# Kernel optimization log

Measured on AMD Instinct MI355X. Metric: run time of the kernel, lower is better.

The kernel has to match this reference:

```python
import jax, jax.numpy as jnp
import numpy as np

B, T, H = 8, 2048, 1024
P = 64           # num_attention_project
N = 4096         # config.n (bias table length), N >= 2T-1
WINDOW = 64      # relative_attention
NEG = -10000.0


def setup_inputs() -> dict:
    key = jax.random.key(0)
    ks = jax.random.split(key, 10)
    s = 1.0 / np.sqrt(H)
    sp = 1.0 / np.sqrt(P)
    sb = 1.0 / np.sqrt(N)
    return {
        "attn_input": jax.random.normal(ks[0], (B, T, H), dtype=jnp.float32),
        "attention_mask": jnp.ones((B, T), dtype=jnp.float32),
        # Linear weights stored as [in, out] so y = x @ W + b
        "Wq": jax.random.uniform(ks[1], (H, P), minval=-s, maxval=s),
        "bq": jnp.zeros((P,), jnp.float32),
        "Wk": jax.random.uniform(ks[2], (H, P), minval=-s, maxval=s),
        "bk": jnp.zeros((P,), jnp.float32),
        "Wv": jax.random.uniform(ks[3], (H, P), minval=-s, maxval=s),
        "bv": jnp.zeros((P,), jnp.float32),
        "Wo": jax.random.uniform(ks[4], (P, H), minval=-sp, maxval=sp),
        "bo": jnp.zeros((H,), jnp.float32),
        "bias": jax.random.uniform(ks[5], (N,), minval=-sb, maxval=sb),
    }


def reference(attn_input, attention_mask, Wq, bq, Wk, bk, Wv, bv, Wo, bo, bias):
    q = attn_input @ Wq + bq            # [B,T,P]
    k = attn_input @ Wk + bk
    v = attn_input @ Wv + bv
    scores = jnp.einsum("btp,bsp->bts", q, k) / jnp.sqrt(jnp.float32(P))  # [B,T,T]
    # padding mask: note original broadcasts over COLUMNS via unsqueeze(-1)
    scores = scores + (1.0 - attention_mask)[:, :, None] * NEG
    # circulant window mask: keep |i-j| <= WINDOW (all ones if WINDOW >= T)
    i = jnp.arange(T)
    rel = i[:, None] - i[None, :]       # i - j
    win = (jnp.abs(rel) <= WINDOW) | (WINDOW >= T)
    scores = scores + jnp.where(win, 0.0, NEG)[None, :, :]
    # gathered learnable relative-position bias: bias[n//2 - i + j]
    scores = scores + bias[N // 2 - rel][None, :, :]
    attn = jax.nn.softmax(scores, axis=-1)
    out = jnp.einsum("bts,bsp->btp", attn, v)
    return out @ Wo + bo                # [B,T,H]
```

## Files before the change

kernel.cpp:

```cpp
#include <hip/hip_runtime.h>

using bf16x8 = __attribute__((ext_vector_type(8))) short;
using f32x4  = __attribute__((ext_vector_type(4))) float;

static __device__ inline unsigned short f2bf(float f) {
  unsigned int u = __float_as_uint(f);
  u += 0x7fffu + ((u >> 16) & 1u);
  return (unsigned short)(u >> 16);
}
static __device__ inline unsigned int pk2(float a, float b) {
  return (unsigned int)f2bf(a) | ((unsigned int)f2bf(b) << 16);
}

#define BAR_LGKM() { asm volatile("s_waitcnt lgkmcnt(0)" ::: "memory"); \
                     __builtin_amdgcn_sched_barrier(0); \
                     __builtin_amdgcn_s_barrier(); }

#define ROW16_MAX(x) { \
  { int _t = __builtin_amdgcn_update_dpp(0, __float_as_int(x), 0x121, 0xf, 0xf, true); x = fmaxf(x, __int_as_float(_t)); } \
  { int _t = __builtin_amdgcn_update_dpp(0, __float_as_int(x), 0x122, 0xf, 0xf, true); x = fmaxf(x, __int_as_float(_t)); } \
  { int _t = __builtin_amdgcn_update_dpp(0, __float_as_int(x), 0x124, 0xf, 0xf, true); x = fmaxf(x, __int_as_float(_t)); } \
  { int _t = __builtin_amdgcn_update_dpp(0, __float_as_int(x), 0x128, 0xf, 0xf, true); x = fmaxf(x, __int_as_float(_t)); } }
#define ROW16_SUM(x) { \
  { int _t = __builtin_amdgcn_update_dpp(0, __float_as_int(x), 0x121, 0xf, 0xf, true); x += __int_as_float(_t); } \
  { int _t = __builtin_amdgcn_update_dpp(0, __float_as_int(x), 0x122, 0xf, 0xf, true); x += __int_as_float(_t); } \
  { int _t = __builtin_amdgcn_update_dpp(0, __float_as_int(x), 0x124, 0xf, 0xf, true); x += __int_as_float(_t); } \
  { int _t = __builtin_amdgcn_update_dpp(0, __float_as_int(x), 0x128, 0xf, 0xf, true); x += __int_as_float(_t); } }

__global__ __launch_bounds__(256) void prep_kernel(
    const float* __restrict__ Wq, const float* __restrict__ Wk, const float* __restrict__ Wv,
    const float* __restrict__ Wo, const float* __restrict__ bq, const float* __restrict__ bk,
    const float* __restrict__ bv,
    unsigned short* __restrict__ Wt, unsigned short* __restrict__ Wot, float* __restrict__ bqkv)
{
  int idx = blockIdx.x * 256 + threadIdx.x;
  if (idx < 192 * 1024) {
    int n = idx >> 10, k = idx & 1023;
    const float* W = (n < 64) ? Wq : (n < 128) ? Wk : Wv;
    Wt[idx] = f2bf(W[k * 64 + (n & 63)]);
  } else if (idx < 192 * 1024 + 1024 * 64) {
    int j = idx - 192 * 1024;
    int n = j >> 6, k = j & 63;
    Wot[j] = f2bf(Wo[k * 1024 + n]);
  } else if (idx < 192 * 1024 + 1024 * 64 + 192) {
    int n = idx - (192 * 1024 + 1024 * 64);
    bqkv[n] = (n < 64) ? bq[n] : (n < 128) ? bk[n - 64] : bv[n - 128];
  }
}

union __align__(16) SharedU {
  struct { unsigned short A[2][192 * 72]; unsigned short B[2][192 * 72]; } p1;
  struct {
    unsigned short Qs[64 * 72];
    unsigned short Kl[192 * 72];
    unsigned short Vt[64 * 216];
    unsigned short Ps[4 * 16 * 168];
    unsigned short Obf[64 * 72];
    float Osum[4][16][64];
    float Mx[8][16];
    float Lx[8][16];
    float biasL[129];
  } p2;
};

#define MLOAD(KS, F0, F1, BB) { \
  _Pragma("unroll") \
  for (int i_ = 0; i_ < 3; ++i_) { \
    const float* a_ = srcA[i_] + (KS) * 64; \
    F0[i_] = *(const float4*)a_; F1[i_] = *(const float4*)(a_ + 4); \
    BB[i_] = *(const uint4*)(srcB[i_] + (KS) * 64); } }

#define MSTORE(BUF, F0, F1, BB) { \
  _Pragma("unroll") \
  for (int i_ = 0; i_ < 3; ++i_) { \
    uint4 p_; \
    p_.x = pk2(F0[i_].x, F0[i_].y); p_.y = pk2(F0[i_].z, F0[i_].w); \
    p_.z = pk2(F1[i_].x, F1[i_].y); p_.w = pk2(F1[i_].z, F1[i_].w); \
    *(uint4*)(sh.p1.A[BUF] + (i_ * 64 + tr) * 72 + cA * 8) = p_; \
    *(uint4*)(sh.p1.B[BUF] + (i_ * 64 + tr) * 72 + cA * 8) = BB[i_]; } }

#define MMMA(BUF) { \
  _Pragma("unroll") \
  for (int kk = 0; kk < 64; kk += 32) { \
    int ko = kk + quad * 8; \
    bf16x8 bfr[3]; \
    _Pragma("unroll") \
    for (int nt = 0; nt < 3; ++nt) \
      bfr[nt] = *(const bf16x8*)(sh.p1.B[BUF] + ((wn * 3 + nt) * 16 + col) * 72 + ko); \
    _Pragma("unroll") \
    for (int mt = 0; mt < 6; ++mt) { \
      bf16x8 afr = *(const bf16x8*)(sh.p1.A[BUF] + ((wm * 6 + mt) * 16 + col) * 72 + ko); \
      _Pragma("unroll") \
      for (int nt = 0; nt < 3; ++nt) \
        acc[mt][nt] = __builtin_amdgcn_mfma_f32_16x16x32_bf16(afr, bfr[nt], acc[mt][nt], 0, 0, 0); \
    } } }

__global__ __launch_bounds__(512, 2) void fused_attn(
    const float* __restrict__ X, const unsigned short* __restrict__ Wt,
    const float* __restrict__ bqkv, const float* __restrict__ bias,
    const unsigned short* __restrict__ Wot, const float* __restrict__ bo,
    float* __restrict__ out)
{
  __shared__ SharedU sh;
  int t = threadIdx.x;
  int lane = t & 63, w = t >> 6;
  int col = lane & 15, quad = lane >> 4, q4 = quad * 4;
  int bidx = blockIdx.x;
  int b = bidx >> 5;
  int i0 = (bidx & 31) * 64;
  const float* xbase = X + (size_t)(b << 11) * 1024;

  int wm = w >> 2, wn = w & 3;
  f32x4 acc[6][3] = {};
  int tr = t >> 3, cA = t & 7;
  const float* srcA[3];
  const unsigned short* srcB[3];
  #pragma unroll
  for (int i = 0; i < 3; ++i) {
    int row = i * 64 + tr;
    int jb = i0 - 64 + row;
    int jc = jb < 0 ? 0 : (jb > 2047 ? 2047 : jb);
    srcA[i] = xbase + (size_t)jc * 1024 + cA * 8;
    srcB[i] = Wt + (size_t)row * 1024 + cA * 8;
  }
  float bov[3];
  #pragma unroll
  for (int nt = 0; nt < 3; ++nt) bov[nt] = bqkv[wn * 48 + nt * 16 + col];

  float4 eF0[3], eF1[3]; uint4 eB[3];
  float4 oF0[3], oF1[3]; uint4 oB[3];
  MLOAD(0, eF0, eF1, eB);
  MLOAD(1, oF0, oF1, oB);
  for (int ks = 0; ks < 16; ks += 2) {
    MSTORE(0, eF0, eF1, eB);
    if (ks + 2 < 16) MLOAD(ks + 2, eF0, eF1, eB);
    BAR_LGKM();
    MMMA(0);
    MSTORE(1, oF0, oF1, oB);
    if (ks + 3 < 16) MLOAD(ks + 3, oF0, oF1, oB);
    BAR_LGKM();
    MMMA(1);
  }
  BAR_LGKM();

  const unsigned short* wb_base = Wot + (size_t)(w * 128 + col) * 64 + quad * 8;
  bf16x8 wb[8][2];
  #pragma unroll
  for (int ns = 0; ns < 8; ++ns) {
    wb[ns][0] = *(const bf16x8*)(wb_base + ns * 16 * 64);
    wb[ns][1] = *(const bf16x8*)(wb_base + ns * 16 * 64 + 32);
  }
  float bov8[8];
  #pragma unroll
  for (int ns = 0; ns < 8; ++ns) bov8[ns] = bo[w * 128 + ns * 16 + col];

  if (t < 129) sh.p2.biasL[t] = bias[1984 + t];
  #pragma unroll
  for (int mt = 0; mt < 6; ++mt) {
    #pragma unroll
    for (int nt = 0; nt < 3; ++nt) {
      int n = wn * 48 + nt * 16 + col;
      #pragma unroll
      for (int r = 0; r < 4; ++r) {
        int m = wm * 96 + mt * 16 + q4 + r;
        unsigned short h = f2bf(acc[mt][nt][r] + bov[nt]);
        if (n < 64) {
          bool isq = (wm == 0) ? (mt >= 4) : (mt < 2);
          if (isq) sh.p2.Qs[(m - 64) * 72 + n] = h;
        } else if (n < 128) {
          sh.p2.Kl[m * 72 + (n - 64)] = h;
        } else {
          sh.p2.Vt[(n - 128) * 216 + m] = h;
        }
      }
    }
  }
  if (t < 256) {
    int pz = t >> 2, c0 = 192 + (t & 3) * 4;
    *(uint2*)(sh.p2.Vt + pz * 216 + c0) = make_uint2(0u, 0u);
  }
  BAR_LGKM();

  int p = w >> 1, s = w & 1;
  int iq = i0 + p * 16;
  bf16x8 aq0 = *(const bf16x8*)(sh.p2.Qs + (p * 16 + col) * 72 + quad * 8);
  bf16x8 aq1 = *(const bf16x8*)(sh.p2.Qs + (p * 16 + col) * 72 + 32 + quad * 8);

  int nt9 = 5 - s, t9b = 5 * s;
  f32x4 sv[5];
  for (int i = 0; i < nt9; ++i) {
    int t9 = t9b + i;
    int krow = ((p + t9) * 16 + col) * 72;
    bf16x8 kb0 = *(const bf16x8*)(sh.p2.Kl + krow + quad * 8);
    bf16x8 kb1 = *(const bf16x8*)(sh.p2.Kl + krow + 32 + quad * 8);
    f32x4 z = {};
    z = __builtin_amdgcn_mfma_f32_16x16x32_bf16(aq0, kb0, z, 0, 0, 0);
    sv[i] = __builtin_amdgcn_mfma_f32_16x16x32_bf16(aq1, kb1, z, 0, 0, 0);
  }
  float mrow[4] = {-3e38f, -3e38f, -3e38f, -3e38f};
  for (int i = 0; i < nt9; ++i) {
    int t9 = t9b + i;
    int j = iq - 64 + t9 * 16 + col;
    #pragma unroll
    for (int r = 0; r < 4; ++r) {
      int diff = q4 + r + 64 - t9 * 16 - col;
      bool valid = (j >= 0) & (j < 2048) & (diff >= -64) & (diff <= 64);
      int bi = 64 - diff; bi = bi < 0 ? 0 : (bi > 128 ? 128 : bi);
      float x = valid ? (sv[i][r] * 0.125f + sh.p2.biasL[bi]) : -3e38f;
      sv[i][r] = x;
      mrow[r] = fmaxf(mrow[r], x);
    }
  }
  #pragma unroll
  for (int r = 0; r < 4; ++r) ROW16_MAX(mrow[r]);
  if (col == 0) {
    #pragma unroll
    for (int r = 0; r < 4; ++r) sh.p2.Mx[w][q4 + r] = mrow[r];
  }
  BAR_LGKM();
  #pragma unroll
  for (int r = 0; r < 4; ++r) mrow[r] = fmaxf(mrow[r], sh.p2.Mx[w ^ 1][q4 + r]);

  unsigned short* Pw = sh.p2.Ps + p * (16 * 168);
  float lsum[4] = {0.f, 0.f, 0.f, 0.f};
  for (int i = 0; i < nt9; ++i) {
    int t9 = t9b + i;
    #pragma unroll
    for (int r = 0; r < 4; ++r) {
      float pe = __expf(sv[i][r] - mrow[r]);
      lsum[r] += pe;
      Pw[(q4 + r) * 168 + t9 * 16 + col] = f2bf(pe);
    }
  }
  #pragma unroll
  for (int r = 0; r < 4; ++r) ROW16_SUM(lsum[r]);
  if (col == 0) {
    #pragma unroll
    for (int r = 0; r < 4; ++r) sh.p2.Lx[w][q4 + r] = lsum[r];
  }
  if (s == 0) {
    #pragma unroll
    for (int r = 0; r < 4; ++r) Pw[(q4 + r) * 168 + 144 + col] = 0;
  }
  BAR_LGKM();
  #pragma unroll
  for (int r = 0; r < 4; ++r) lsum[r] += sh.p2.Lx[w ^ 1][q4 + r];

  f32x4 o[4] = {};
  int nkc = 3 - s, kcb = 3 * s;
  for (int i = 0; i < nkc; ++i) {
    int kc = kcb + i;
    bf16x8 pa = *(const bf16x8*)(Pw + col * 168 + kc * 32 + quad * 8);
    #pragma unroll
    for (int nt = 0; nt < 4; ++nt) {
      bf16x8 vb = *(const bf16x8*)(sh.p2.Vt + (nt * 16 + col) * 216 + 16 * p + kc * 32 + quad * 8);
      o[nt] = __builtin_amdgcn_mfma_f32_16x16x32_bf16(pa, vb, o[nt], 0, 0, 0);
    }
  }
  if (s == 1) {
    #pragma unroll
    for (int nt = 0; nt < 4; ++nt)
      #pragma unroll
      for (int r = 0; r < 4; ++r)
        sh.p2.Osum[p][q4 + r][nt * 16 + col] = o[nt][r];
  }
  BAR_LGKM();
  if (s == 0) {
    float rl[4];
    #pragma unroll
    for (int r = 0; r < 4; ++r) rl[r] = 1.0f / lsum[r];
    #pragma unroll
    for (int nt = 0; nt < 4; ++nt)
      #pragma unroll
      for (int r = 0; r < 4; ++r)
        sh.p2.Obf[(p * 16 + q4 + r) * 72 + nt * 16 + col] =
            f2bf((o[nt][r] + sh.p2.Osum[p][q4 + r][nt * 16 + col]) * rl[r]);
  }
  BAR_LGKM();

  float* outbase = out + ((size_t)(b << 11) + i0) * 1024 + w * 128;
  #pragma unroll
  for (int mt = 0; mt < 4; ++mt) {
    bf16x8 a0 = *(const bf16x8*)(sh.p2.Obf + (mt * 16 + col) * 72 + quad * 8);
    bf16x8 a1 = *(const bf16x8*)(sh.p2.Obf + (mt * 16 + col) * 72 + 32 + quad * 8);
    f32x4 acc8[8] = {};
    #pragma unroll
    for (int ns = 0; ns < 8; ++ns) {
      acc8[ns] = __builtin_amdgcn_mfma_f32_16x16x32_bf16(a0, wb[ns][0], acc8[ns], 0, 0, 0);
      acc8[ns] = __builtin_amdgcn_mfma_f32_16x16x32_bf16(a1, wb[ns][1], acc8[ns], 0, 0, 0);
    }
    #pragma unroll
    for (int ns = 0; ns < 8; ++ns)
      #pragma unroll
      for (int r = 0; r < 4; ++r)
        outbase[(size_t)(mt * 16 + q4 + r) * 1024 + ns * 16 + col] = acc8[ns][r] + bov8[ns];
  }
}

extern "C" void kernel_launch(void* const* d_in, const int* in_sizes, int n_in,
                              void* d_out, int out_size, void* d_ws, size_t ws_size,
                              hipStream_t stream) {
  const float* X    = (const float*)d_in[0];
  const float* Wq   = (const float*)d_in[2];
  const float* bq   = (const float*)d_in[3];
  const float* Wk   = (const float*)d_in[4];
  const float* bk   = (const float*)d_in[5];
  const float* Wv   = (const float*)d_in[6];
  const float* bv   = (const float*)d_in[7];
  const float* Wo   = (const float*)d_in[8];
  const float* bo   = (const float*)d_in[9];
  const float* bias = (const float*)d_in[10];
  float* out = (float*)d_out;
  char* ws = (char*)d_ws;
  unsigned short* Wt   = (unsigned short*)(ws);
  unsigned short* Wot  = (unsigned short*)(ws + 393216);
  float*          bqkv = (float*)(ws + 524288);

  prep_kernel<<<1025, 256, 0, stream>>>(Wq, Wk, Wv, Wo, bq, bk, bv, Wt, Wot, bqkv);
  fused_attn<<<256, 512, 0, stream>>>(X, Wt, bqkv, bias, Wot, bo, out);
}
```

Measured before the change: 175.5 us.

## Shrink shared memory and registers to raise occupancy in fused attention

The QKV projection loop now stages 32-wide K slices with single-step prefetch instead of 64-wide double-buffered pairs, which shrinks LDS and prefetch registers. The attention-phase buffers are aliased into a manually laid-out shared region, with Q, P and the normalized output reusing one buffer. The PV product is split over output columns instead of the key dimension, removing the cross-wave Osum reduction. The Wo fragment loads move after attention to cut live registers. Launch bounds now request 4 blocks per CU, and a block-index swizzle interleaves batches. The cost is twice as many barriers in the projection loop and a shallower load prefetch.

```diff
diff --git a/kernel.cpp b/kernel.cpp
--- a/kernel.cpp
+++ b/kernel.cpp
@@ -48,113 +48,86 @@
   }
 }
 
-union __align__(16) SharedU {
-  struct { unsigned short A[2][192 * 72]; unsigned short B[2][192 * 72]; } p1;
-  struct {
-    unsigned short Qs[64 * 72];
-    unsigned short Kl[192 * 72];
-    unsigned short Vt[64 * 216];
-    unsigned short Ps[4 * 16 * 168];
-    unsigned short Obf[64 * 72];
-    float Osum[4][16][64];
-    float Mx[8][16];
-    float Lx[8][16];
-    float biasL[129];
-  } p2;
-};
-
-#define MLOAD(KS, F0, F1, BB) { \
-  _Pragma("unroll") \
-  for (int i_ = 0; i_ < 3; ++i_) { \
-    const float* a_ = srcA[i_] + (KS) * 64; \
-    F0[i_] = *(const float4*)a_; F1[i_] = *(const float4*)(a_ + 4); \
-    BB[i_] = *(const uint4*)(srcB[i_] + (KS) * 64); } }
-
-#define MSTORE(BUF, F0, F1, BB) { \
-  _Pragma("unroll") \
-  for (int i_ = 0; i_ < 3; ++i_) { \
-    uint4 p_; \
-    p_.x = pk2(F0[i_].x, F0[i_].y); p_.y = pk2(F0[i_].z, F0[i_].w); \
-    p_.z = pk2(F1[i_].x, F1[i_].y); p_.w = pk2(F1[i_].z, F1[i_].w); \
-    *(uint4*)(sh.p1.A[BUF] + (i_ * 64 + tr) * 72 + cA * 8) = p_; \
-    *(uint4*)(sh.p1.B[BUF] + (i_ * 64 + tr) * 72 + cA * 8) = BB[i_]; } }
-
-#define MMMA(BUF) { \
-  _Pragma("unroll") \
-  for (int kk = 0; kk < 64; kk += 32) { \
-    int ko = kk + quad * 8; \
-    bf16x8 bfr[3]; \
-    _Pragma("unroll") \
-    for (int nt = 0; nt < 3; ++nt) \
-      bfr[nt] = *(const bf16x8*)(sh.p1.B[BUF] + ((wn * 3 + nt) * 16 + col) * 72 + ko); \
-    _Pragma("unroll") \
-    for (int mt = 0; mt < 6; ++mt) { \
-      bf16x8 afr = *(const bf16x8*)(sh.p1.A[BUF] + ((wm * 6 + mt) * 16 + col) * 72 + ko); \
-      _Pragma("unroll") \
-      for (int nt = 0; nt < 3; ++nt) \
-        acc[mt][nt] = __builtin_amdgcn_mfma_f32_16x16x32_bf16(afr, bfr[nt], acc[mt][nt], 0, 0, 0); \
-    } } }
-
-__global__ __launch_bounds__(512, 2) void fused_attn(
+__global__ __launch_bounds__(512, 4) void fused_attn(
     const float* __restrict__ X, const unsigned short* __restrict__ Wt,
     const float* __restrict__ bqkv, const float* __restrict__ bias,
     const unsigned short* __restrict__ Wot, const float* __restrict__ bo,
     float* __restrict__ out)
 {
-  __shared__ SharedU sh;
+  __shared__ __align__(16) char smem[78848];
+  unsigned short* const Kl  = (unsigned short*)(smem);
+  unsigned short* const Vt  = (unsigned short*)(smem + 27648);
+  unsigned short* const PsU = (unsigned short*)(smem + 55296);
+  float* const Mx    = (float*)(smem + 76800);
+  float* const Lx    = (float*)(smem + 77312);
+  float* const biasL = (float*)(smem + 77824);
+  unsigned short* const As_ = (unsigned short*)(smem);
+  unsigned short* const Bs_ = (unsigned short*)(smem + 30720);
+
   int t = threadIdx.x;
   int lane = t & 63, w = t >> 6;
   int col = lane & 15, quad = lane >> 4, q4 = quad * 4;
-  int bidx = blockIdx.x;
-  int b = bidx >> 5;
-  int i0 = (bidx & 31) * 64;
+  int L = ((blockIdx.x & 7) << 5) | (blockIdx.x >> 3);
+  int b = L >> 5;
+  int i0 = (L & 31) * 64;
   const float* xbase = X + (size_t)(b << 11) * 1024;
+
+  if (t < 129) biasL[t] = bias[1984 + t];
 
   int wm = w >> 2, wn = w & 3;
   f32x4 acc[6][3] = {};
-  int tr = t >> 3, cA = t & 7;
-  const float* srcA[3];
-  const unsigned short* srcB[3];
+  int tr = t >> 3, c4 = t & 7;
+  int offA[3], offB[3];
   #pragma unroll
   for (int i = 0; i < 3; ++i) {
     int row = i * 64 + tr;
     int jb = i0 - 64 + row;
     int jc = jb < 0 ? 0 : (jb > 2047 ? 2047 : jb);
-    srcA[i] = xbase + (size_t)jc * 1024 + cA * 8;
-    srcB[i] = Wt + (size_t)row * 1024 + cA * 8;
+    offA[i] = jc * 1024 + c4 * 4;
+    offB[i] = row * 1024 + c4 * 4;
   }
   float bov[3];
   #pragma unroll
   for (int nt = 0; nt < 3; ++nt) bov[nt] = bqkv[wn * 48 + nt * 16 + col];
 
-  float4 eF0[3], eF1[3]; uint4 eB[3];
-  float4 oF0[3], oF1[3]; uint4 oB[3];
-  MLOAD(0, eF0, eF1, eB);
-  MLOAD(1, oF0, oF1, oB);
-  for (int ks = 0; ks < 16; ks += 2) {
-    MSTORE(0, eF0, eF1, eB);
-    if (ks + 2 < 16) MLOAD(ks + 2, eF0, eF1, eB);
+  float4 pA[3]; uint2 pB[3];
+  #pragma unroll
+  for (int i = 0; i < 3; ++i) {
+    pA[i] = *(const float4*)(xbase + offA[i]);
+    pB[i] = *(const uint2*)(Wt + offB[i]);
+  }
+  for (int ks = 0; ks < 32; ++ks) {
+    unsigned short* A  = As_ + (ks & 1) * 7680;
+    unsigned short* Bb = Bs_ + (ks & 1) * 7680;
+    #pragma unroll
+    for (int i = 0; i < 3; ++i) {
+      *(uint2*)(A  + (i * 64 + tr) * 40 + c4 * 4) =
+          make_uint2(pk2(pA[i].x, pA[i].y), pk2(pA[i].z, pA[i].w));
+      *(uint2*)(Bb + (i * 64 + tr) * 40 + c4 * 4) = pB[i];
+    }
+    if (ks + 1 < 32) {
+      #pragma unroll
+      for (int i = 0; i < 3; ++i) {
+        pA[i] = *(const float4*)(xbase + offA[i] + (ks + 1) * 32);
+        pB[i] = *(const uint2*)(Wt + offB[i] + (ks + 1) * 32);
+      }
+    }
     BAR_LGKM();
-    MMMA(0);
-    MSTORE(1, oF0, oF1, oB);
-    if (ks + 3 < 16) MLOAD(ks + 3, oF0, oF1, oB);
-    BAR_LGKM();
-    MMMA(1);
-  }
-  BAR_LGKM();
-
-  const unsigned short* wb_base = Wot + (size_t)(w * 128 + col) * 64 + quad * 8;
-  bf16x8 wb[8][2];
-  #pragma unroll
-  for (int ns = 0; ns < 8; ++ns) {
-    wb[ns][0] = *(const bf16x8*)(wb_base + ns * 16 * 64);
-    wb[ns][1] = *(const bf16x8*)(wb_base + ns * 16 * 64 + 32);
-  }
-  float bov8[8];
-  #pragma unroll
-  for (int ns = 0; ns < 8; ++ns) bov8[ns] = bo[w * 128 + ns * 16 + col];
-
-  if (t < 129) sh.p2.biasL[t] = bias[1984 + t];
+    int ko = quad * 8;
+    bf16x8 bfr[3];
+    #pragma unroll
+    for (int nt = 0; nt < 3; ++nt)
+      bfr[nt] = *(const bf16x8*)(Bb + ((wn * 3 + nt) * 16 + col) * 40 + ko);
+    #pragma unroll
+    for (int mt = 0; mt < 6; ++mt) {
+      bf16x8 afr = *(const bf16x8*)(A + ((wm * 6 + mt) * 16 + col) * 40 + ko);
+      #pragma unroll
+      for (int nt = 0; nt < 3; ++nt)
+        acc[mt][nt] = __builtin_amdgcn_mfma_f32_16x16x32_bf16(afr, bfr[nt], acc[mt][nt], 0, 0, 0);
+    }
+  }
+  BAR_LGKM();
+
   #pragma unroll
   for (int mt = 0; mt < 6; ++mt) {
     #pragma unroll
@@ -166,33 +139,33 @@
         unsigned short h = f2bf(acc[mt][nt][r] + bov[nt]);
         if (n < 64) {
           bool isq = (wm == 0) ? (mt >= 4) : (mt < 2);
-          if (isq) sh.p2.Qs[(m - 64) * 72 + n] = h;
+          if (isq) PsU[(m - 64) * 72 + n] = h;
         } else if (n < 128) {
-          sh.p2.Kl[m * 72 + (n - 64)] = h;
+          Kl[m * 72 + (n - 64)] = h;
         } else {
-          sh.p2.Vt[(n - 128) * 216 + m] = h;
+          Vt[(n - 128) * 216 + m] = h;
         }
       }
     }
   }
   if (t < 256) {
     int pz = t >> 2, c0 = 192 + (t & 3) * 4;
-    *(uint2*)(sh.p2.Vt + pz * 216 + c0) = make_uint2(0u, 0u);
+    *(uint2*)(Vt + pz * 216 + c0) = make_uint2(0u, 0u);
   }
   BAR_LGKM();
 
   int p = w >> 1, s = w & 1;
   int iq = i0 + p * 16;
-  bf16x8 aq0 = *(const bf16x8*)(sh.p2.Qs + (p * 16 + col) * 72 + quad * 8);
-  bf16x8 aq1 = *(const bf16x8*)(sh.p2.Qs + (p * 16 + col) * 72 + 32 + quad * 8);
+  bf16x8 aq0 = *(const bf16x8*)(PsU + (p * 16 + col) * 72 + quad * 8);
+  bf16x8 aq1 = *(const bf16x8*)(PsU + (p * 16 + col) * 72 + 32 + quad * 8);
 
   int nt9 = 5 - s, t9b = 5 * s;
   f32x4 sv[5];
   for (int i = 0; i < nt9; ++i) {
     int t9 = t9b + i;
     int krow = ((p + t9) * 16 + col) * 72;
-    bf16x8 kb0 = *(const bf16x8*)(sh.p2.Kl + krow + quad * 8);
-    bf16x8 kb1 = *(const bf16x8*)(sh.p2.Kl + krow + 32 + quad * 8);
+    bf16x8 kb0 = *(const bf16x8*)(Kl + krow + quad * 8);
+    bf16x8 kb1 = *(const bf16x8*)(Kl + krow + 32 + quad * 8);
     f32x4 z = {};
     z = __builtin_amdgcn_mfma_f32_16x16x32_bf16(aq0, kb0, z, 0, 0, 0);
     sv[i] = __builtin_amdgcn_mfma_f32_16x16x32_bf16(aq1, kb1, z, 0, 0, 0);
@@ -206,7 +179,7 @@
       int diff = q4 + r + 64 - t9 * 16 - col;
       bool valid = (j >= 0) & (j < 2048) & (diff >= -64) & (diff <= 64);
       int bi = 64 - diff; bi = bi < 0 ? 0 : (bi > 128 ? 128 : bi);
-      float x = valid ? (sv[i][r] * 0.125f + sh.p2.biasL[bi]) : -3e38f;
+      float x = valid ? (sv[i][r] * 0.125f + biasL[bi]) : -3e38f;
       sv[i][r] = x;
       mrow[r] = fmaxf(mrow[r], x);
     }
@@ -215,13 +188,13 @@
   for (int r = 0; r < 4; ++r) ROW16_MAX(mrow[r]);
   if (col == 0) {
     #pragma unroll
-    for (int r = 0; r < 4; ++r) sh.p2.Mx[w][q4 + r] = mrow[r];
-  }
-  BAR_LGKM();
-  #pragma unroll
-  for (int r = 0; r < 4; ++r) mrow[r] = fmaxf(mrow[r], sh.p2.Mx[w ^ 1][q4 + r]);
-
-  unsigned short* Pw = sh.p2.Ps + p * (16 * 168);
+    for (int r = 0; r < 4; ++r) Mx[w * 16 + q4 + r] = mrow[r];
+  }
+  BAR_LGKM();
+  #pragma unroll
+  for (int r = 0; r < 4; ++r) mrow[r] = fmaxf(mrow[r], Mx[(w ^ 1) * 16 + q4 + r]);
+
+  unsigned short* Pw = PsU + p * 2688;
   float lsum[4] = {0.f, 0.f, 0.f, 0.f};
   for (int i = 0; i < nt9; ++i) {
     int t9 = t9b + i;
@@ -236,7 +209,7 @@
   for (int r = 0; r < 4; ++r) ROW16_SUM(lsum[r]);
   if (col == 0) {
     #pragma unroll
-    for (int r = 0; r < 4; ++r) sh.p2.Lx[w][q4 + r] = lsum[r];
+    for (int r = 0; r < 4; ++r) Lx[w * 16 + q4 + r] = lsum[r];
   }
   if (s == 0) {
     #pragma unroll
@@ -244,45 +217,46 @@
   }
   BAR_LGKM();
   #pragma unroll
-  for (int r = 0; r < 4; ++r) lsum[r] += sh.p2.Lx[w ^ 1][q4 + r];
-
-  f32x4 o[4] = {};
-  int nkc = 3 - s, kcb = 3 * s;
-  for (int i = 0; i < nkc; ++i) {
-    int kc = kcb + i;
+  for (int r = 0; r < 4; ++r) lsum[r] += Lx[(w ^ 1) * 16 + q4 + r];
+
+  f32x4 o[2] = {};
+  #pragma unroll
+  for (int kc = 0; kc < 5; ++kc) {
     bf16x8 pa = *(const bf16x8*)(Pw + col * 168 + kc * 32 + quad * 8);
     #pragma unroll
-    for (int nt = 0; nt < 4; ++nt) {
-      bf16x8 vb = *(const bf16x8*)(sh.p2.Vt + (nt * 16 + col) * 216 + 16 * p + kc * 32 + quad * 8);
-      o[nt] = __builtin_amdgcn_mfma_f32_16x16x32_bf16(pa, vb, o[nt], 0, 0, 0);
-    }
-  }
-  if (s == 1) {
-    #pragma unroll
-    for (int nt = 0; nt < 4; ++nt)
+    for (int n2 = 0; n2 < 2; ++n2) {
+      bf16x8 vb = *(const bf16x8*)(Vt + ((s * 2 + n2) * 16 + col) * 216 + 16 * p + kc * 32 + quad * 8);
+      o[n2] = __builtin_amdgcn_mfma_f32_16x16x32_bf16(pa, vb, o[n2], 0, 0, 0);
+    }
+  }
+  BAR_LGKM();
+  {
+    float rl[4];
+    #pragma unroll
+    for (int r = 0; r < 4; ++r) rl[r] = 1.0f / lsum[r];
+    #pragma unroll
+    for (int n2 = 0; n2 < 2; ++n2)
       #pragma unroll
       for (int r = 0; r < 4; ++r)
-        sh.p2.Osum[p][q4 + r][nt * 16 + col] = o[nt][r];
-  }
-  BAR_LGKM();
-  if (s == 0) {
-    float rl[4];
-    #pragma unroll
-    for (int r = 0; r < 4; ++r) rl[r] = 1.0f / lsum[r];
-    #pragma unroll
-    for (int nt = 0; nt < 4; ++nt)
-      #pragma unroll
-      for (int r = 0; r < 4; ++r)
-        sh.p2.Obf[(p * 16 + q4 + r) * 72 + nt * 16 + col] =
-            f2bf((o[nt][r] + sh.p2.Osum[p][q4 + r][nt * 16 + col]) * rl[r]);
-  }
-  BAR_LGKM();
-
+        PsU[(p * 16 + q4 + r) * 72 + s * 32 + n2 * 16 + col] = f2bf(o[n2][r] * rl[r]);
+  }
+  BAR_LGKM();
+
+  const unsigned short* wb_base = Wot + (size_t)(w * 128 + col) * 64 + quad * 8;
+  bf16x8 wb[8][2];
+  #pragma unroll
+  for (int ns = 0; ns < 8; ++ns) {
+    wb[ns][0] = *(const bf16x8*)(wb_base + ns * 16 * 64);
+    wb[ns][1] = *(const bf16x8*)(wb_base + ns * 16 * 64 + 32);
+  }
+  float bov8[8];
+  #pragma unroll
+  for (int ns = 0; ns < 8; ++ns) bov8[ns] = bo[w * 128 + ns * 16 + col];
   float* outbase = out + ((size_t)(b << 11) + i0) * 1024 + w * 128;
   #pragma unroll
   for (int mt = 0; mt < 4; ++mt) {
-    bf16x8 a0 = *(const bf16x8*)(sh.p2.Obf + (mt * 16 + col) * 72 + quad * 8);
-    bf16x8 a1 = *(const bf16x8*)(sh.p2.Obf + (mt * 16 + col) * 72 + 32 + quad * 8);
+    bf16x8 a0 = *(const bf16x8*)(PsU + (mt * 16 + col) * 72 + quad * 8);
+    bf16x8 a1 = *(const bf16x8*)(PsU + (mt * 16 + col) * 72 + 32 + quad * 8);
     f32x4 acc8[8] = {};
     #pragma unroll
     for (int ns = 0; ns < 8; ++ns) {
```

After: 192.3 us. +9.6%, slower.
